# Performance work log

Hardware: AMD Instinct MI355X
Metric: run time of the kernel (lower is better)

The kernel has to match this reference:

```python
import jax, jax.numpy as jnp
import numpy as np

T = 5
NORM_GROUPS = 4
EPS = 1e-5


def setup_inputs() -> dict:
    key = jax.random.key(0)
    inputs = jax.random.normal(key, (16384, 2048), dtype=jnp.float32)
    return {"inputs": inputs}


def reference(inputs):
    k = inputs.shape
    C = k[-1]
    g = NORM_GROUPS
    d = C // g
    # (g, N, d) where N = total_elems / C * ... = fan_in for a 2D weight
    Z = inputs.reshape(g, -1, d)
    Zc = Z - jnp.mean(Z, axis=1, keepdims=True)           # center over samples
    S = jnp.einsum('gnd,gne->gde', Zc, Zc)                # (g, d, d) covariance
    eye = jnp.eye(d, dtype=inputs.dtype)[None]            # (1, d, d)
    S = S + EPS * eye
    norm_S = jnp.sqrt(jnp.sum(S * S, axis=(1, 2), keepdims=True))  # Frobenius
    S = S / norm_S
    # Newton-Schulz iterations: B_{t+1} = 1.5 B_t - 0.5 B_t^3 S
    B = jnp.broadcast_to(eye, S.shape)
    for _ in range(T):
        B3 = (B @ B) @ B
        B = 1.5 * B - 0.5 * (B3 @ S)
    # W = B Zc^T / sqrt(||S||_F)  -> (g, d, N)
    W = (B @ jnp.swapaxes(Zc, 1, 2)) / jnp.sqrt(norm_S)
    return jnp.swapaxes(W, 1, 2).reshape(k)
```

## Files before the change

### kernel.cpp

```cpp
#include <hip/hip_runtime.h>
#include <hip/hip_bf16.h>

#define NG 4
#define DD 512
#define NN 16384
#define EPSV 1e-5f
#define GRP_ELEMS ((size_t)NN * DD)
#define MAT_ELEMS ((size_t)DD * DD)
#define KCHUNKS 8

typedef __attribute__((ext_vector_type(8))) short bf16x8;
typedef __attribute__((ext_vector_type(4))) float f32x4;

__device__ __forceinline__ ushort f2b(float f) {
    union { float f; unsigned u; } x; x.f = f;
    unsigned r = (x.u + 0x7fffu + ((x.u >> 16) & 1u)) >> 16;
    return (ushort)r;
}
__device__ __forceinline__ float b2f(ushort u) {
    union { unsigned u; float f; } x; x.u = ((unsigned)u) << 16;
    return x.f;
}
__device__ __forceinline__ void load_lds16(const ushort* g, ushort* l) {
    __builtin_amdgcn_global_load_lds(
        (const __attribute__((address_space(1))) void*)g,
        (__attribute__((address_space(3))) void*)l, 16, 0, 0);
}

__global__ __launch_bounds__(256) void convT_kernel(const float* __restrict__ Z,
                                                    ushort* __restrict__ ZbT,
                                                    ushort* __restrict__ Zb,
                                                    float* __restrict__ csP) {
    __shared__ float tile[64][65];
    int g = blockIdx.z;
    int n0 = blockIdx.x * 64;
    int d0 = blockIdx.y * 64;
    int t = threadIdx.x;
    int c4 = (t & 15) * 4;
    int r = t >> 4;
    const float* Zg = Z + (size_t)g * GRP_ELEMS;
    ushort* ZbG = Zb + (size_t)g * GRP_ELEMS;
    #pragma unroll
    for (int p = 0; p < 4; ++p) {
        int rr = r + p * 16;
        float4 v = *(const float4*)&Zg[(size_t)(n0 + rr) * DD + d0 + c4];
        tile[rr][c4 + 0] = v.x;
        tile[rr][c4 + 1] = v.y;
        tile[rr][c4 + 2] = v.z;
        tile[rr][c4 + 3] = v.w;
        ushort4 o;
        o.x = f2b(v.x); o.y = f2b(v.y); o.z = f2b(v.z); o.w = f2b(v.w);
        *(ushort4*)&ZbG[(size_t)(n0 + rr) * DD + d0 + c4] = o;
    }
    __syncthreads();
    ushort* Og = ZbT + (size_t)g * GRP_ELEMS;
    #pragma unroll
    for (int p = 0; p < 4; ++p) {
        int dl = r + p * 16;
        int nl = c4;
        ushort4 o;
        o.x = f2b(tile[nl + 0][dl]);
        o.y = f2b(tile[nl + 1][dl]);
        o.z = f2b(tile[nl + 2][dl]);
        o.w = f2b(tile[nl + 3][dl]);
        *(ushort4*)&Og[(size_t)(d0 + dl) * NN + n0 + nl] = o;
    }
    if (t < 64) {
        float s = 0.f;
        #pragma unroll 8
        for (int n = 0; n < 64; ++n) s += tile[n][t];
        csP[((size_t)g * 256 + blockIdx.x) * 512 + d0 + t] = s;
    }
}

__global__ __launch_bounds__(256) void colsum_fin(const float* __restrict__ csP,
                                                  float* __restrict__ cs) {
    int c = blockIdx.x * 256 + threadIdx.x;
    int g = c >> 9, d = c & 511;
    const float* p = csP + (size_t)g * 256 * 512 + d;
    float s = 0.f;
    #pragma unroll 8
    for (int b = 0; b < 256; ++b) s += p[(size_t)b * 512];
    cs[c] = s * (1.f / (float)NN);
}

template<int MODE>
__global__ __launch_bounds__(256) void gemm_bt(
    const ushort* __restrict__ Ap, const ushort* __restrict__ Bp,
    float* __restrict__ outF, ushort* __restrict__ outU,
    const ushort* __restrict__ Curp, const float* __restrict__ nrm,
    const float* __restrict__ bmup,
    int Mtiles, int lda, int ldb, int K, size_t grpA, size_t grpB)
{
    __shared__ __align__(16) ushort As[128 * 32];
    __shared__ __align__(16) ushort Bs[128 * 32];
    const int g = blockIdx.z;
    const int tm = (blockIdx.x % Mtiles) * 128;
    const int tn = (blockIdx.x / Mtiles) * 128;
    const int kstart = blockIdx.y * K;
    const ushort* Ag = Ap + (size_t)g * grpA;
    const ushort* Bg = Bp + (size_t)g * grpB;
    const int t = threadIdx.x;
    const int wave = t >> 6, lane = t & 63;
    const int lr = lane >> 2;
    const int lc = (lane & 3) * 8;
    const int s0 = wave * 2;
    const int qm = (wave & 1) * 64, qn = (wave >> 1) * 64;
    const int fm = lane & 15;
    const int fk = (lane >> 4) * 8;

    const ushort* a0p = Ag + (size_t)(tm + s0 * 16 + lr) * lda + lc;
    const ushort* a1p = Ag + (size_t)(tm + s0 * 16 + 16 + lr) * lda + lc;
    const ushort* b0p = Bg + (size_t)(tn + s0 * 16 + lr) * ldb + lc;
    const ushort* b1p = Bg + (size_t)(tn + s0 * 16 + 16 + lr) * ldb + lc;
    ushort* lA0 = As + s0 * 512;
    ushort* lA1 = As + s0 * 512 + 512;
    ushort* lB0 = Bs + s0 * 512;
    ushort* lB1 = Bs + s0 * 512 + 512;

    f32x4 acc[4][4] = {};
    for (int k0 = kstart; k0 < kstart + K; k0 += 32) {
        load_lds16(a0p + k0, lA0);
        load_lds16(a1p + k0, lA1);
        load_lds16(b0p + k0, lB0);
        load_lds16(b1p + k0, lB1);
        __syncthreads();
        bf16x8 af[4], bfr[4];
        #pragma unroll
        for (int i = 0; i < 4; ++i) {
            af[i]  = *(const bf16x8*)&As[(qm + i * 16 + fm) * 32 + fk];
            bfr[i] = *(const bf16x8*)&Bs[(qn + i * 16 + fm) * 32 + fk];
        }
        #pragma unroll
        for (int i = 0; i < 4; ++i)
            #pragma unroll
            for (int j = 0; j < 4; ++j)
                acc[i][j] = __builtin_amdgcn_mfma_f32_16x16x32_bf16(
                    af[i], bfr[j], acc[i][j], 0, 0, 0);
        __syncthreads();
    }

    const int cn0 = tn + qn + fm;
    const int cm0 = tm + qm + (lane >> 4) * 4;
    if (MODE == 0) {
        float* O = outF + (size_t)(blockIdx.y * NG + g) * MAT_ELEMS;
        #pragma unroll
        for (int i = 0; i < 4; ++i)
            #pragma unroll
            for (int r = 0; r < 4; ++r) {
                size_t row = (size_t)(cm0 + i * 16 + r) * DD;
                #pragma unroll
                for (int j = 0; j < 4; ++j)
                    O[row + cn0 + j * 16] = acc[i][j][r];
            }
    } else if (MODE == 1) {
        ushort* O = outU + (size_t)g * MAT_ELEMS;
        #pragma unroll
        for (int i = 0; i < 4; ++i)
            #pragma unroll
            for (int r = 0; r < 4; ++r) {
                size_t row = (size_t)(cm0 + i * 16 + r) * DD;
                #pragma unroll
                for (int j = 0; j < 4; ++j)
                    O[row + cn0 + j * 16] = f2b(acc[i][j][r]);
            }
    } else if (MODE == 2) {
        const ushort* C = Curp + (size_t)g * MAT_ELEMS;
        ushort* O = outU + (size_t)g * MAT_ELEMS;
        float sc = 0.5f * rsqrtf(nrm[g]);
        #pragma unroll
        for (int i = 0; i < 4; ++i)
            #pragma unroll
            for (int r = 0; r < 4; ++r) {
                size_t row = (size_t)(cm0 + i * 16 + r) * DD;
                #pragma unroll
                for (int j = 0; j < 4; ++j) {
                    size_t off = row + cn0 + j * 16;
                    O[off] = f2b(1.5f * b2f(C[off]) - sc * acc[i][j][r]);
                }
            }
    } else {
        float* O = outF + (size_t)g * GRP_ELEMS;
        float sc = rsqrtf(sqrtf(nrm[g]));
        const float* bm = bmup + g * DD;
        float bmj[4];
        #pragma unroll
        for (int j = 0; j < 4; ++j) bmj[j] = bm[cn0 + j * 16];
        #pragma unroll
        for (int i = 0; i < 4; ++i)
            #pragma unroll
            for (int r = 0; r < 4; ++r) {
                size_t row = (size_t)(cm0 + i * 16 + r) * DD;
                #pragma unroll
                for (int j = 0; j < 4; ++j)
                    O[row + cn0 + j * 16] = sc * (acc[i][j][r] - bmj[j]);
            }
    }
}

__global__ __launch_bounds__(256) void reduce_fin(const float* __restrict__ Sp,
                                                  const float* __restrict__ cs,
                                                  ushort* __restrict__ Sb,
                                                  float* __restrict__ nrmP) {
    __shared__ float wsum[4];
    int g = blockIdx.z;
    int idx = blockIdx.x * 256 + threadIdx.x;
    float v = 0.f;
    #pragma unroll
    for (int c = 0; c < KCHUNKS; ++c)
        v += Sp[(size_t)(c * NG + g) * MAT_ELEMS + idx];
    int i = idx >> 9, j = idx & 511;
    v -= (float)NN * cs[g * DD + i] * cs[g * DD + j];
    if (i == j) v += EPSV;
    Sb[(size_t)g * MAT_ELEMS + idx] = f2b(v);
    float ss = v * v;
    #pragma unroll
    for (int o = 32; o; o >>= 1) ss += __shfl_down(ss, o, 64);
    if ((threadIdx.x & 63) == 0) wsum[threadIdx.x >> 6] = ss;
    __syncthreads();
    if (threadIdx.x == 0)
        nrmP[(size_t)g * 1024 + blockIdx.x] = wsum[0] + wsum[1] + wsum[2] + wsum[3];
}

__global__ __launch_bounds__(256) void nrm_fin(const float* __restrict__ nrmP,
                                               float* __restrict__ nrm) {
    __shared__ float wsum[4];
    int g = blockIdx.x;
    float s = 0.f;
    #pragma unroll
    for (int p = 0; p < 4; ++p)
        s += nrmP[(size_t)g * 1024 + p * 256 + threadIdx.x];
    #pragma unroll
    for (int o = 32; o; o >>= 1) s += __shfl_down(s, o, 64);
    if ((threadIdx.x & 63) == 0) wsum[threadIdx.x >> 6] = s;
    __syncthreads();
    if (threadIdx.x == 0) nrm[g] = wsum[0] + wsum[1] + wsum[2] + wsum[3];
}

__global__ __launch_bounds__(256) void initB_kernel(const ushort* __restrict__ Sb,
                                                    const float* __restrict__ nrm,
                                                    ushort* __restrict__ B0) {
    int g = blockIdx.z;
    int idx = blockIdx.x * 256 + threadIdx.x;
    int i = idx >> 9, j = idx & 511;
    float invnu = rsqrtf(nrm[g]);
    size_t off = (size_t)g * MAT_ELEMS + idx;
    float v = ((i == j) ? 1.5f : 0.f) - 0.5f * invnu * b2f(Sb[off]);
    B0[off] = f2b(v);
}

__global__ __launch_bounds__(256) void bmu_kernel(const ushort* __restrict__ B,
                                                  const float* __restrict__ cs,
                                                  float* __restrict__ bmu) {
    int g = blockIdx.z;
    int wave = threadIdx.x >> 6, lane = threadIdx.x & 63;
    int i = blockIdx.x * 4 + wave;
    const ushort* Bg = B + (size_t)g * MAT_ELEMS + (size_t)i * DD + lane * 8;
    const float* mu = cs + g * DD + lane * 8;
    ushort4 u0 = *(const ushort4*)(Bg);
    ushort4 u1 = *(const ushort4*)(Bg + 4);
    float s = b2f(u0.x) * mu[0] + b2f(u0.y) * mu[1]
            + b2f(u0.z) * mu[2] + b2f(u0.w) * mu[3]
            + b2f(u1.x) * mu[4] + b2f(u1.y) * mu[5]
            + b2f(u1.z) * mu[6] + b2f(u1.w) * mu[7];
    #pragma unroll
    for (int o = 32; o; o >>= 1) s += __shfl_down(s, o, 64);
    if (lane == 0) bmu[g * DD + i] = s;
}

extern "C" void kernel_launch(void* const* d_in, const int* in_sizes, int n_in,
                              void* d_out, int out_size, void* d_ws, size_t ws_size,
                              hipStream_t stream) {
    const float* Z = (const float*)d_in[0];
    float* out = (float*)d_out;
    float* ws = (float*)d_ws;

    float* cs   = ws;
    float* nrm  = ws + 2048;
    float* bmu  = ws + 2112;
    float* nrmP = ws + 4160;
    float* csP  = ws + 8256;
    ushort* ZbT = (ushort*)(ws + 532544);
    ushort* Zb  = (ushort*)(ws + 17309760);
    float* Spart = ws + 34086976;
    ushort* Sb = (ushort*)(Spart + (size_t)KCHUNKS * NG * MAT_ELEMS);
    ushort* B0 = Sb + NG * MAT_ELEMS;
    ushort* B1 = B0 + NG * MAT_ELEMS;
    ushort* Pb = B1 + NG * MAT_ELEMS;
    ushort* Qb = Pb + NG * MAT_ELEMS;

    convT_kernel<<<dim3(256, 8, NG), 256, 0, stream>>>(Z, ZbT, Zb, csP);
    colsum_fin<<<dim3(8), 256, 0, stream>>>(csP, cs);

    gemm_bt<0><<<dim3(16, KCHUNKS, NG), 256, 0, stream>>>(
        ZbT, ZbT, Spart, nullptr, nullptr, nullptr, nullptr,
        4, NN, NN, NN / KCHUNKS, GRP_ELEMS, GRP_ELEMS);

    reduce_fin<<<dim3(1024, 1, NG), 256, 0, stream>>>(Spart, cs, Sb, nrmP);
    nrm_fin<<<dim3(NG), 256, 0, stream>>>(nrmP, nrm);

    initB_kernel<<<dim3(1024, 1, NG), 256, 0, stream>>>(Sb, nrm, B0);

    ushort* cur = B0; ushort* nxt = B1;
    for (int it = 0; it < 4; ++it) {
        gemm_bt<1><<<dim3(16, 1, NG), 256, 0, stream>>>(
            cur, cur, nullptr, Pb, nullptr, nullptr, nullptr,
            4, DD, DD, DD, MAT_ELEMS, MAT_ELEMS);
        gemm_bt<1><<<dim3(16, 1, NG), 256, 0, stream>>>(
            Pb, cur, nullptr, Qb, nullptr, nullptr, nullptr,
            4, DD, DD, DD, MAT_ELEMS, MAT_ELEMS);
        gemm_bt<2><<<dim3(16, 1, NG), 256, 0, stream>>>(
            Qb, Sb, nullptr, nxt, cur, nrm, nullptr,
            4, DD, DD, DD, MAT_ELEMS, MAT_ELEMS);
        ushort* tmp = cur; cur = nxt; nxt = tmp;
    }

    bmu_kernel<<<dim3(128, 1, NG), 256, 0, stream>>>(cur, cs, bmu);

    gemm_bt<3><<<dim3(512, 1, NG), 256, 0, stream>>>(
        Zb, cur, out, nullptr, nullptr, nrm, bmu,
        128, DD, DD, DD, GRP_ELEMS, MAT_ELEMS);
}
```

Measured before the change: 553.1 us.

## Widen transpose tiles, halve K-split, and fuse Newton-Schulz GEMM pair into one launch

```diff
diff --git a/kernel.cpp b/kernel.cpp
--- a/kernel.cpp
+++ b/kernel.cpp
@@ -7,7 +7,7 @@
 #define EPSV 1e-5f
 #define GRP_ELEMS ((size_t)NN * DD)
 #define MAT_ELEMS ((size_t)DD * DD)
-#define KCHUNKS 8
+#define KCHUNKS 4
 
 typedef __attribute__((ext_vector_type(8))) short bf16x8;
 typedef __attribute__((ext_vector_type(4))) float f32x4;
@@ -31,45 +31,49 @@
                                                     ushort* __restrict__ ZbT,
                                                     ushort* __restrict__ Zb,
                                                     float* __restrict__ csP) {
-    __shared__ float tile[64][65];
+    __shared__ __align__(16) unsigned tileT[64][132];
     int g = blockIdx.z;
-    int n0 = blockIdx.x * 64;
+    int n0 = blockIdx.x * 256;
     int d0 = blockIdx.y * 64;
     int t = threadIdx.x;
-    int c4 = (t & 15) * 4;
-    int r = t >> 4;
+    int k4 = (t & 15) * 4;
+    int q = t >> 4;
     const float* Zg = Z + (size_t)g * GRP_ELEMS;
     ushort* ZbG = Zb + (size_t)g * GRP_ELEMS;
     #pragma unroll
-    for (int p = 0; p < 4; ++p) {
-        int rr = r + p * 16;
-        float4 v = *(const float4*)&Zg[(size_t)(n0 + rr) * DD + d0 + c4];
-        tile[rr][c4 + 0] = v.x;
-        tile[rr][c4 + 1] = v.y;
-        tile[rr][c4 + 2] = v.z;
-        tile[rr][c4 + 3] = v.w;
-        ushort4 o;
-        o.x = f2b(v.x); o.y = f2b(v.y); o.z = f2b(v.z); o.w = f2b(v.w);
-        *(ushort4*)&ZbG[(size_t)(n0 + rr) * DD + d0 + c4] = o;
+    for (int p = 0; p < 8; ++p) {
+        int np = q + 16 * p;
+        size_t r0 = (size_t)(n0 + 2 * np) * DD + d0 + k4;
+        float4 va = *(const float4*)&Zg[r0];
+        float4 vb = *(const float4*)&Zg[r0 + DD];
+        ushort4 oa, ob;
+        oa.x = f2b(va.x); oa.y = f2b(va.y); oa.z = f2b(va.z); oa.w = f2b(va.w);
+        ob.x = f2b(vb.x); ob.y = f2b(vb.y); ob.z = f2b(vb.z); ob.w = f2b(vb.w);
+        *(ushort4*)&ZbG[r0] = oa;
+        *(ushort4*)&ZbG[r0 + DD] = ob;
+        tileT[k4 + 0][np] = (unsigned)oa.x | ((unsigned)ob.x << 16);
+        tileT[k4 + 1][np] = (unsigned)oa.y | ((unsigned)ob.y << 16);
+        tileT[k4 + 2][np] = (unsigned)oa.z | ((unsigned)ob.z << 16);
+        tileT[k4 + 3][np] = (unsigned)oa.w | ((unsigned)ob.w << 16);
     }
     __syncthreads();
     ushort* Og = ZbT + (size_t)g * GRP_ELEMS;
     #pragma unroll
-    for (int p = 0; p < 4; ++p) {
-        int dl = r + p * 16;
-        int nl = c4;
-        ushort4 o;
-        o.x = f2b(tile[nl + 0][dl]);
-        o.y = f2b(tile[nl + 1][dl]);
-        o.z = f2b(tile[nl + 2][dl]);
-        o.w = f2b(tile[nl + 3][dl]);
-        *(ushort4*)&Og[(size_t)(d0 + dl) * NN + n0 + nl] = o;
+    for (int pp = 0; pp < 8; ++pp) {
+        int ci = pp * 256 + t;
+        int r = ci >> 5;
+        int c = ci & 31;
+        uint4 v = *(const uint4*)&tileT[r][c * 4];
+        *(uint4*)&Og[(size_t)(d0 + r) * NN + n0 + c * 8] = v;
     }
     if (t < 64) {
         float s = 0.f;
-        #pragma unroll 8
-        for (int n = 0; n < 64; ++n) s += tile[n][t];
-        csP[((size_t)g * 256 + blockIdx.x) * 512 + d0 + t] = s;
+        #pragma unroll 16
+        for (int j = 0; j < 128; ++j) {
+            unsigned u = tileT[t][j];
+            s += b2f((ushort)(u & 0xffffu)) + b2f((ushort)(u >> 16));
+        }
+        csP[((size_t)g * 64 + blockIdx.x) * 512 + d0 + t] = s;
     }
 }
 
@@ -77,10 +81,10 @@
                                                   float* __restrict__ cs) {
     int c = blockIdx.x * 256 + threadIdx.x;
     int g = c >> 9, d = c & 511;
-    const float* p = csP + (size_t)g * 256 * 512 + d;
+    const float* p = csP + (size_t)g * 64 * 512 + d;
     float s = 0.f;
     #pragma unroll 8
-    for (int b = 0; b < 256; ++b) s += p[(size_t)b * 512];
+    for (int b = 0; b < 64; ++b) s += p[(size_t)b * 512];
     cs[c] = s * (1.f / (float)NN);
 }
 
@@ -90,16 +94,22 @@
     float* __restrict__ outF, ushort* __restrict__ outU,
     const ushort* __restrict__ Curp, const float* __restrict__ nrm,
     const float* __restrict__ bmup,
+    const ushort* __restrict__ Bp2, ushort* __restrict__ outU2,
     int Mtiles, int lda, int ldb, int K, size_t grpA, size_t grpB)
 {
     __shared__ __align__(16) ushort As[128 * 32];
     __shared__ __align__(16) ushort Bs[128 * 32];
     const int g = blockIdx.z;
-    const int tm = (blockIdx.x % Mtiles) * 128;
-    const int tn = (blockIdx.x / Mtiles) * 128;
+    int bx = blockIdx.x;
+    int half = 0;
+    if (MODE == 4) { half = bx >> 4; bx &= 15; }
+    const ushort* Bsrc = (MODE == 4 && half) ? Bp2 : Bp;
+    ushort* Udst = (MODE == 4 && half) ? outU2 : outU;
+    const int tm = (bx % Mtiles) * 128;
+    const int tn = (bx / Mtiles) * 128;
     const int kstart = blockIdx.y * K;
     const ushort* Ag = Ap + (size_t)g * grpA;
-    const ushort* Bg = Bp + (size_t)g * grpB;
+    const ushort* Bg = Bsrc + (size_t)g * grpB;
     const int t = threadIdx.x;
     const int wave = t >> 6, lane = t & 63;
     const int lr = lane >> 2;
@@ -153,8 +163,8 @@
                 for (int j = 0; j < 4; ++j)
                     O[row + cn0 + j * 16] = acc[i][j][r];
             }
-    } else if (MODE == 1) {
-        ushort* O = outU + (size_t)g * MAT_ELEMS;
+    } else if (MODE == 1 || MODE == 4) {
+        ushort* O = Udst + (size_t)g * MAT_ELEMS;
         #pragma unroll
         for (int i = 0; i < 4; ++i)
             #pragma unroll
@@ -280,20 +290,20 @@
     float* bmu  = ws + 2112;
     float* nrmP = ws + 4160;
     float* csP  = ws + 8256;
-    ushort* ZbT = (ushort*)(ws + 532544);
-    ushort* Zb  = (ushort*)(ws + 17309760);
-    float* Spart = ws + 34086976;
+    ushort* ZbT = (ushort*)(ws + 139328);
+    ushort* Zb  = ZbT + NG * GRP_ELEMS;
+    float* Spart = (float*)(Zb + NG * GRP_ELEMS);
     ushort* Sb = (ushort*)(Spart + (size_t)KCHUNKS * NG * MAT_ELEMS);
     ushort* B0 = Sb + NG * MAT_ELEMS;
     ushort* B1 = B0 + NG * MAT_ELEMS;
     ushort* Pb = B1 + NG * MAT_ELEMS;
     ushort* Qb = Pb + NG * MAT_ELEMS;
 
-    convT_kernel<<<dim3(256, 8, NG), 256, 0, stream>>>(Z, ZbT, Zb, csP);
+    convT_kernel<<<dim3(64, 8, NG), 256, 0, stream>>>(Z, ZbT, Zb, csP);
     colsum_fin<<<dim3(8), 256, 0, stream>>>(csP, cs);
 
     gemm_bt<0><<<dim3(16, KCHUNKS, NG), 256, 0, stream>>>(
-        ZbT, ZbT, Spart, nullptr, nullptr, nullptr, nullptr,
+        ZbT, ZbT, Spart, nullptr, nullptr, nullptr, nullptr, nullptr, nullptr,
         4, NN, NN, NN / KCHUNKS, GRP_ELEMS, GRP_ELEMS);
 
     reduce_fin<<<dim3(1024, 1, NG), 256, 0, stream>>>(Spart, cs, Sb, nrmP);
@@ -303,14 +313,11 @@
 
     ushort* cur = B0; ushort* nxt = B1;
     for (int it = 0; it < 4; ++it) {
-        gemm_bt<1><<<dim3(16, 1, NG), 256, 0, stream>>>(
-            cur, cur, nullptr, Pb, nullptr, nullptr, nullptr,
-            4, DD, DD, DD, MAT_ELEMS, MAT_ELEMS);
-        gemm_bt<1><<<dim3(16, 1, NG), 256, 0, stream>>>(
-            Pb, cur, nullptr, Qb, nullptr, nullptr, nullptr,
+        gemm_bt<4><<<dim3(32, 1, NG), 256, 0, stream>>>(
+            cur, cur, nullptr, Pb, nullptr, nullptr, nullptr, Sb, Qb,
             4, DD, DD, DD, MAT_ELEMS, MAT_ELEMS);
         gemm_bt<2><<<dim3(16, 1, NG), 256, 0, stream>>>(
-            Qb, Sb, nullptr, nxt, cur, nrm, nullptr,
+            Pb, Qb, nullptr, nxt, cur, nrm, nullptr, nullptr, nullptr,
             4, DD, DD, DD, MAT_ELEMS, MAT_ELEMS);
         ushort* tmp = cur; cur = nxt; nxt = tmp;
     }
@@ -318,6 +325,6 @@
     bmu_kernel<<<dim3(128, 1, NG), 256, 0, stream>>>(cur, cs, bmu);
 
     gemm_bt<3><<<dim3(512, 1, NG), 256, 0, stream>>>(
-        Zb, cur, out, nullptr, nullptr, nrm, bmu,
+        Zb, cur, out, nullptr, nullptr, nrm, bmu, nullptr, nullptr,
         128, DD, DD, DD, GRP_ELEMS, MAT_ELEMS);
 }
```

Result: faster. 533.1 us (-3.6%).
